# Kernel tuning notes

Hardware: AMD Instinct MI355X
Metric: run time of the kernel (lower is better)

## Reference

```python
import jax, jax.numpy as jnp
import numpy as np

H_UPPER = 10  # module is in steady-state branch (h_count > h_upper)


def setup_inputs() -> dict:
    key = jax.random.key(0)
    k1, k2, k3 = jax.random.split(key, 3)
    B, D = 2048, 16384
    h = jax.random.normal(k1, (B, D), dtype=jnp.float32)
    h_mean = jax.random.normal(k2, (1, D), dtype=jnp.float32)
    h_var = jax.random.uniform(k3, (1, D), dtype=jnp.float32)  # positive running variance
    return {"h": h, "h_mean": h_mean, "h_var": h_var}


def reference(h, h_mean, h_var):
    B = h.shape[0]
    U = H_UPPER
    # --- running-stat update (stats computed on detached h) ---
    h_d = jax.lax.stop_gradient(h)
    h_u = jnp.mean(h_d, axis=0, keepdims=True)            # [1, D]
    h_v = jnp.var(h_d, axis=0, keepdims=True)             # unbiased=False, [1, D]
    new_var = (h_var * (U - 1.0 / B) + h_v + (h_u - h_mean) ** 2 / (1.0 + 1.0 / U)) / (U + 1.0 - 1.0 / B)
    new_mean = (h_mean * U + h_u) / (U + 1.0)
    # --- punish_best: per-row top-1 normalized deviation, select-and-scatter ---
    denom = new_var + jnp.mean(new_var) / 100.0           # [1, D]
    scores = (h - new_mean) ** 2 / denom                  # [B, D]
    flat = h.reshape(B, -1)
    idx = jnp.argmax(scores.reshape(B, -1), axis=1)       # [B] winning column per row
    rows = jnp.arange(B)
    change = jnp.zeros_like(flat).at[rows, idx].set(1.0)  # one-hot mask
    mean_f = new_mean.reshape(-1)
    sel_detached = jax.lax.stop_gradient(flat)[rows, idx]
    inc = jnp.zeros_like(flat).at[rows, idx].set(mean_f[idx] + sel_detached)
    out = (1.0 - 2.0 * change) * flat + inc               # winner -> running mean (grad -1 path)
    return out.reshape(h.shape)
```

## Files before the change

kernel.cpp:

```cpp
#include <hip/hip_runtime.h>


namespace {

constexpr int B = 2048;
constexpr int D = 16384;
constexpr int NCHUNK = 32;
constexpr int ROWS_PER_CHUNK = B / NCHUNK;
constexpr int COLBLKS = D / 1024;

__global__ __launch_bounds__(256) void k1_colstats(const float* __restrict__ h,
                                                   float* __restrict__ ps,
                                                   float* __restrict__ pq) {
    const int colblk = blockIdx.x & (COLBLKS - 1);
    const int chunk  = blockIdx.x >> 4;
    const int c0 = colblk * 1024 + threadIdx.x * 4;
    const float* base = h + (size_t)(chunk * ROWS_PER_CHUNK) * D + c0;
    float4 s = make_float4(0.f, 0.f, 0.f, 0.f);
    float4 q = make_float4(0.f, 0.f, 0.f, 0.f);
#pragma unroll 8
    for (int r = 0; r < ROWS_PER_CHUNK; ++r) {
        float4 v = *reinterpret_cast<const float4*>(base + (size_t)r * D);
        s.x += v.x; s.y += v.y; s.z += v.z; s.w += v.w;
        q.x = fmaf(v.x, v.x, q.x);
        q.y = fmaf(v.y, v.y, q.y);
        q.z = fmaf(v.z, v.z, q.z);
        q.w = fmaf(v.w, v.w, q.w);
    }
    *reinterpret_cast<float4*>(ps + chunk * D + c0) = s;
    *reinterpret_cast<float4*>(pq + chunk * D + c0) = q;
}

__global__ __launch_bounds__(256) void k2_colfinal(const float* __restrict__ ps,
                                                   const float* __restrict__ pq,
                                                   const float* __restrict__ h_mean,
                                                   const float* __restrict__ h_var,
                                                   float* __restrict__ nm,
                                                   float* __restrict__ nv,
                                                   float* __restrict__ bsum) {
    const int d = blockIdx.x * 256 + threadIdx.x;
    float s = 0.f, q = 0.f;
#pragma unroll
    for (int c = 0; c < NCHUNK; ++c) {
        s += ps[c * D + d];
        q += pq[c * D + d];
    }
    constexpr float invB = 1.0f / (float)B;
    const float hu = s * invB;
    const float hv = q * invB - hu * hu;
    const float hm  = h_mean[d];
    const float hvr = h_var[d];
    const float du  = hu - hm;
    const float newvar  = (hvr * (10.0f - invB) + hv + (du * du) / 1.1f) / (11.0f - invB);
    const float newmean = (hm * 10.0f + hu) / 11.0f;
    nm[d] = newmean;
    nv[d] = newvar;

    __shared__ float red[256];
    red[threadIdx.x] = newvar;
    __syncthreads();
#pragma unroll
    for (int off = 128; off > 0; off >>= 1) {
        if (threadIdx.x < off) red[threadIdx.x] += red[threadIdx.x + off];
        __syncthreads();
    }
    if (threadIdx.x == 0) bsum[blockIdx.x] = red[0];
}

__global__ __launch_bounds__(256) void k2c_invden(const float* __restrict__ nv,
                                                  const float* __restrict__ bsum,
                                                  float* __restrict__ invden) {
    __shared__ float red[64];
    if (threadIdx.x < 64) red[threadIdx.x] = bsum[threadIdx.x];
    __syncthreads();
#pragma unroll
    for (int off = 32; off > 0; off >>= 1) {
        if (threadIdx.x < off) red[threadIdx.x] += red[threadIdx.x + off];
        __syncthreads();
    }
    const float c = (red[0] / (float)D) / 100.0f;
    const int d = blockIdx.x * 256 + threadIdx.x;
    invden[d] = 1.0f / (nv[d] + c);
}

__global__ __launch_bounds__(256) void k3_punish(const float* __restrict__ h,
                                                 const float* __restrict__ nm,
                                                 const float* __restrict__ invden,
                                                 float* __restrict__ out) {
    const int row = blockIdx.x;
    const float* hrow = h + (size_t)row * D;
    float* orow = out + (size_t)row * D;

    float best = -1.0f;
    int bidx = 0;
#pragma unroll
    for (int i = 0; i < 16; ++i) {
        const int c = i * 1024 + threadIdx.x * 4;
        const float4 v = *reinterpret_cast<const float4*>(hrow + c);
        const float4 m = *reinterpret_cast<const float4*>(nm + c);
        const float4 w = *reinterpret_cast<const float4*>(invden + c);
        *reinterpret_cast<float4*>(orow + c) = v;
        const float dx = v.x - m.x, dy = v.y - m.y, dz = v.z - m.z, dw = v.w - m.w;
        const float sx = dx * dx * w.x;
        const float sy = dy * dy * w.y;
        const float sz = dz * dz * w.z;
        const float sw = dw * dw * w.w;
        if (sx > best) { best = sx; bidx = c + 0; }
        if (sy > best) { best = sy; bidx = c + 1; }
        if (sz > best) { best = sz; bidx = c + 2; }
        if (sw > best) { best = sw; bidx = c + 3; }
    }

    __shared__ float ss[256];
    __shared__ int   si[256];
    ss[threadIdx.x] = best;
    si[threadIdx.x] = bidx;
    __syncthreads();
#pragma unroll
    for (int off = 128; off > 0; off >>= 1) {
        if (threadIdx.x < off) {
            const float so = ss[threadIdx.x + off];
            const int   io = si[threadIdx.x + off];
            if (so > ss[threadIdx.x] || (so == ss[threadIdx.x] && io < si[threadIdx.x])) {
                ss[threadIdx.x] = so;
                si[threadIdx.x] = io;
            }
        }
        __syncthreads();
    }
    if (threadIdx.x == 0) {
        const int widx = si[0];
        orow[widx] = nm[widx];
    }
}

}

extern "C" void kernel_launch(void* const* d_in, const int* in_sizes, int n_in,
                              void* d_out, int out_size, void* d_ws, size_t ws_size,
                              hipStream_t stream) {
    const float* h      = (const float*)d_in[0];
    const float* h_mean = (const float*)d_in[1];
    const float* h_var  = (const float*)d_in[2];
    float* out = (float*)d_out;

    float* ws  = (float*)d_ws;
    float* ps  = ws;
    float* pq  = ps + NCHUNK * D;
    float* nm  = pq + NCHUNK * D;
    float* nv  = nm + D;
    float* inv = nv + D;
    float* bsum = inv + D;

    k1_colstats<<<NCHUNK * COLBLKS, 256, 0, stream>>>(h, ps, pq);
    k2_colfinal<<<D / 256, 256, 0, stream>>>(ps, pq, h_mean, h_var, nm, nv, bsum);
    k2c_invden<<<D / 256, 256, 0, stream>>>(nv, bsum, inv);
    k3_punish<<<B, 256, 0, stream>>>(h, nm, inv, out);
}
```

Before: 270.4 us.

## Fuse four kernels into one cooperative kernel with grid-wide syncs

Replaces the four separate launches (column stats, column finalize, inverse denominator, per-row argmax scatter) with a single cooperative kernel of 512 blocks that uses grid.sync between phases. Each block then handles four rows in the punish phase. The aim is to remove launch gaps and inter-kernel drain between the small phases. In exchange, the final phase has only 512 blocks looping serially over rows, which limits latency hiding, and three grid barriers are added. If the cooperative launch fails, the original four kernels run instead.

```diff
diff --git a/kernel.cpp b/kernel.cpp
--- a/kernel.cpp
+++ b/kernel.cpp
@@ -1,4 +1,5 @@
 #include <hip/hip_runtime.h>
+#include <hip/hip_cooperative_groups.h>
 
 
 namespace {
@@ -8,13 +9,16 @@
 constexpr int NCHUNK = 32;
 constexpr int ROWS_PER_CHUNK = B / NCHUNK;
 constexpr int COLBLKS = D / 1024;
-
-__global__ __launch_bounds__(256) void k1_colstats(const float* __restrict__ h,
-                                                   float* __restrict__ ps,
-                                                   float* __restrict__ pq) {
-    const int colblk = blockIdx.x & (COLBLKS - 1);
-    const int chunk  = blockIdx.x >> 4;
-    const int c0 = colblk * 1024 + threadIdx.x * 4;
+constexpr int GRID = NCHUNK * COLBLKS;
+constexpr int ROWS_PER_BLOCK = B / GRID;
+
+__device__ __forceinline__ void phaseA(const float* __restrict__ h,
+                                       float* __restrict__ ps,
+                                       float* __restrict__ pq,
+                                       int bid, int tid) {
+    const int colblk = bid & (COLBLKS - 1);
+    const int chunk  = bid >> 4;
+    const int c0 = colblk * 1024 + tid * 4;
     const float* base = h + (size_t)(chunk * ROWS_PER_CHUNK) * D + c0;
     float4 s = make_float4(0.f, 0.f, 0.f, 0.f);
     float4 q = make_float4(0.f, 0.f, 0.f, 0.f);
@@ -29,6 +33,125 @@
     }
     *reinterpret_cast<float4*>(ps + chunk * D + c0) = s;
     *reinterpret_cast<float4*>(pq + chunk * D + c0) = q;
+}
+
+__global__ __launch_bounds__(256) void kfused(const float* __restrict__ h,
+                                              const float* __restrict__ h_mean,
+                                              const float* __restrict__ h_var,
+                                              float* __restrict__ out,
+                                              float* __restrict__ ps,
+                                              float* __restrict__ pq,
+                                              float* __restrict__ nm,
+                                              float* __restrict__ nv,
+                                              float* __restrict__ inv,
+                                              float* __restrict__ bsum) {
+    cooperative_groups::grid_group grid = cooperative_groups::this_grid();
+    const int tid = threadIdx.x;
+    const int bid = blockIdx.x;
+
+    __shared__ float red[256];
+    __shared__ float ss[256];
+    __shared__ int   si[256];
+
+    phaseA(h, ps, pq, bid, tid);
+    grid.sync();
+
+    if (bid < 64) {
+        const int d = bid * 256 + tid;
+        float s = 0.f, q = 0.f;
+#pragma unroll
+        for (int c = 0; c < NCHUNK; ++c) {
+            s += ps[c * D + d];
+            q += pq[c * D + d];
+        }
+        constexpr float invB = 1.0f / (float)B;
+        const float hu = s * invB;
+        const float hv = q * invB - hu * hu;
+        const float hm  = h_mean[d];
+        const float hvr = h_var[d];
+        const float du  = hu - hm;
+        const float newvar  = (hvr * (10.0f - invB) + hv + (du * du) / 1.1f) / (11.0f - invB);
+        const float newmean = (hm * 10.0f + hu) / 11.0f;
+        nm[d] = newmean;
+        nv[d] = newvar;
+
+        red[tid] = newvar;
+        __syncthreads();
+#pragma unroll
+        for (int off = 128; off > 0; off >>= 1) {
+            if (tid < off) red[tid] += red[tid + off];
+            __syncthreads();
+        }
+        if (tid == 0) bsum[bid] = red[0];
+    }
+    grid.sync();
+
+    if (bid < 64) {
+        if (tid < 64) red[tid] = bsum[tid];
+        __syncthreads();
+#pragma unroll
+        for (int off = 32; off > 0; off >>= 1) {
+            if (tid < off) red[tid] += red[tid + off];
+            __syncthreads();
+        }
+        const float c = (red[0] / (float)D) / 100.0f;
+        const int d = bid * 256 + tid;
+        inv[d] = 1.0f / (nv[d] + c);
+    }
+    grid.sync();
+
+    for (int rr = 0; rr < ROWS_PER_BLOCK; ++rr) {
+        const int row = bid * ROWS_PER_BLOCK + rr;
+        const float* hrow = h + (size_t)row * D;
+        float* orow = out + (size_t)row * D;
+
+        float best = -1.0f;
+        int bidx = 0;
+#pragma unroll
+        for (int i = 0; i < 16; ++i) {
+            const int c = i * 1024 + tid * 4;
+            const float4 v = *reinterpret_cast<const float4*>(hrow + c);
+            const float4 m = *reinterpret_cast<const float4*>(nm + c);
+            const float4 w = *reinterpret_cast<const float4*>(inv + c);
+            *reinterpret_cast<float4*>(orow + c) = v;
+            const float dx = v.x - m.x, dy = v.y - m.y, dz = v.z - m.z, dw = v.w - m.w;
+            const float sx = dx * dx * w.x;
+            const float sy = dy * dy * w.y;
+            const float sz = dz * dz * w.z;
+            const float sw = dw * dw * w.w;
+            if (sx > best) { best = sx; bidx = c + 0; }
+            if (sy > best) { best = sy; bidx = c + 1; }
+            if (sz > best) { best = sz; bidx = c + 2; }
+            if (sw > best) { best = sw; bidx = c + 3; }
+        }
+
+        ss[tid] = best;
+        si[tid] = bidx;
+        __syncthreads();
+#pragma unroll
+        for (int off = 128; off > 0; off >>= 1) {
+            if (tid < off) {
+                const float so = ss[tid + off];
+                const int   io = si[tid + off];
+                if (so > ss[tid] || (so == ss[tid] && io < si[tid])) {
+                    ss[tid] = so;
+                    si[tid] = io;
+                }
+            }
+            __syncthreads();
+        }
+        if (tid == 0) {
+            const int widx = si[0];
+            orow[widx] = nm[widx];
+        }
+        __syncthreads();
+    }
+}
+
+__global__ __launch_bounds__(256) void k1_colstats(const float* __restrict__ h,
+                                                   float* __restrict__ ps,
+                                                   float* __restrict__ pq) {
+    phaseA(h, ps, pq, blockIdx.x, threadIdx.x);
 }
 
 __global__ __launch_bounds__(256) void k2_colfinal(const float* __restrict__ ps,
@@ -145,15 +268,22 @@
     float* out = (float*)d_out;
 
     float* ws  = (float*)d_ws;
-    float* ps  = ws;
-    float* pq  = ps + NCHUNK * D;
-    float* nm  = pq + NCHUNK * D;
-    float* nv  = nm + D;
-    float* inv = nv + D;
+    float* ps   = ws;
+    float* pq   = ps + NCHUNK * D;
+    float* nm   = pq + NCHUNK * D;
+    float* nv   = nm + D;
+    float* inv  = nv + D;
     float* bsum = inv + D;
 
-    k1_colstats<<<NCHUNK * COLBLKS, 256, 0, stream>>>(h, ps, pq);
-    k2_colfinal<<<D / 256, 256, 0, stream>>>(ps, pq, h_mean, h_var, nm, nv, bsum);
-    k2c_invden<<<D / 256, 256, 0, stream>>>(nv, bsum, inv);
-    k3_punish<<<B, 256, 0, stream>>>(h, nm, inv, out);
-}
+    void* args[] = {(void*)&h, (void*)&h_mean, (void*)&h_var, (void*)&out,
+                    (void*)&ps, (void*)&pq, (void*)&nm, (void*)&nv,
+                    (void*)&inv, (void*)&bsum};
+    hipError_t err = hipLaunchCooperativeKernel(reinterpret_cast<void*>(kfused),
+                                                dim3(GRID), dim3(256), args, 0, stream);
+    if (err != hipSuccess) {
+        k1_colstats<<<NCHUNK * COLBLKS, 256, 0, stream>>>(h, ps, pq);
+        k2_colfinal<<<D / 256, 256, 0, stream>>>(ps, pq, h_mean, h_var, nm, nv, bsum);
+        k2c_invden<<<D / 256, 256, 0, stream>>>(nv, bsum, inv);
+        k3_punish<<<B, 256, 0, stream>>>(h, nm, inv, out);
+    }
+}
```

After: 445.8 us. +64.9%, slower.
